# Kernel tuning notes

Measured on AMD Instinct MI355X. Metric: run time of the kernel, lower is better.

Reference implementation:

```python
import jax, jax.numpy as jnp
import numpy as np

B, H, W = 8, 384, 384
KH = KW = 3
STRIDE, PAD = 1, 1


def setup_inputs() -> dict:
    key = jax.random.key(0)
    ks = jax.random.split(key, 5)
    pf = jax.random.normal(ks[0], (B, 3, H, W), jnp.float32)
    cf = jax.random.normal(ks[1], (B, 3, H, W), jnp.float32)
    mv = jax.random.normal(ks[2], (B, 2, H, W), jnp.float32)
    offset_w = jax.random.normal(ks[3], (18, 8, KH, KW), jnp.float32) * 0.05
    offset_b = jnp.zeros((18,), jnp.float32)
    deform_w = jax.random.normal(ks[4], (3, 3, KH, KW), jnp.float32) * 0.1
    return dict(pf=pf, cf=cf, mv=mv, offset_w=offset_w, offset_b=offset_b, deform_w=deform_w)


def _conv2d(x, w, b):
    y = jax.lax.conv_general_dilated(
        x, w, window_strides=(STRIDE, STRIDE),
        padding=((PAD, PAD), (PAD, PAD)),
        dimension_numbers=('NCHW', 'OIHW', 'NCHW'))
    return y + b[None, :, None, None]


def _deform_conv2d(x, offset, w):
    # x: [B, Cin, H, W]; offset: [B, 2*KH*KW, Ho, Wo] (torchvision order: per tap k -> (dy, dx))
    Bn, Cin, Hn, Wn = x.shape
    Ho, Wo = offset.shape[2], offset.shape[3]
    K = KH * KW
    off = offset.reshape(Bn, K, 2, Ho, Wo)
    ky = jnp.repeat(jnp.arange(KH), KW).astype(x.dtype)   # [K] kernel row offset
    kx = jnp.tile(jnp.arange(KW), KH).astype(x.dtype)     # [K] kernel col offset
    base_y = (jnp.arange(Ho) * STRIDE - PAD).astype(x.dtype)
    base_x = (jnp.arange(Wo) * STRIDE - PAD).astype(x.dtype)
    # sampling positions p = p0 + p_k + delta_p_k, shape [B, K, Ho, Wo]
    py = off[:, :, 0] + ky[None, :, None, None] + base_y[None, None, :, None]
    px = off[:, :, 1] + kx[None, :, None, None] + base_x[None, None, None, :]
    y0 = jnp.floor(py)
    x0 = jnp.floor(px)
    wy = py - y0  # bilinear weights, [B, K, Ho, Wo]
    wx = px - x0

    def gather(yi, xi):
        # zero padding outside the image (torchvision semantics)
        valid = (yi >= 0) & (yi < Hn) & (xi >= 0) & (xi < Wn)
        yc = jnp.clip(yi, 0, Hn - 1).astype(jnp.int32)
        xc = jnp.clip(xi, 0, Wn - 1).astype(jnp.int32)
        v = jax.vmap(lambda im, y, xg: im[:, y, xg])(x, yc, xc)  # [B, Cin, K, Ho, Wo]
        return v * valid[:, None].astype(x.dtype)

    v00 = gather(y0, x0)
    v01 = gather(y0, x0 + 1)
    v10 = gather(y0 + 1, x0)
    v11 = gather(y0 + 1, x0 + 1)
    wy_ = wy[:, None]  # broadcast over channel dim
    wx_ = wx[:, None]
    samp = (v00 * (1 - wy_) * (1 - wx_) + v01 * (1 - wy_) * wx_
            + v10 * wy_ * (1 - wx_) + v11 * wy_ * wx_)  # [B, Cin, K, Ho, Wo]
    # weighted accumulation over taps and input channels (no bias)
    return jnp.einsum('oik,bikhw->bohw', w.reshape(w.shape[0], w.shape[1], K), samp)


def reference(pf, cf, mv, offset_w, offset_b, deform_w):
    x = jnp.concatenate([pf, cf, mv], axis=1)          # [B, 8, H, W]
    offset = _conv2d(x, offset_w, offset_b)            # [B, 18, H, W]
    return _deform_conv2d(pf, offset, deform_w)        # [B, 3, H, W]
```

## Files before the change

kernel.cpp:

```cpp
#include <hip/hip_runtime.h>


#define Bn 8
#define Hn 384
#define Wn 384
#define HWn (Hn * Wn)
#define TILE 16
#define PH 4
#define PT 24

#define OFF_PTILE 0
#define SZ_PTILE (PT * PT * 2)
#define OFF_T8   SZ_PTILE
#define SZ_T8U   4864
#define SMEM_FLOATS (OFF_T8 + SZ_T8U)

typedef float f32x4 __attribute__((ext_vector_type(4)));
typedef float f32x2 __attribute__((ext_vector_type(2)));
typedef unsigned u32x2 __attribute__((ext_vector_type(2)));
typedef short s16x8 __attribute__((ext_vector_type(8)));

static __device__ inline f32x2 vfma2(f32x2 a, f32x2 b, f32x2 c) {
#if __has_builtin(__builtin_elementwise_fma)
    return __builtin_elementwise_fma(a, b, c);
#else
    f32x2 r; r.x = fmaf(a.x, b.x, c.x); r.y = fmaf(a.y, b.y, c.y); return r;
#endif
}
static __device__ inline f32x2 vfloor2(f32x2 a) {
#if __has_builtin(__builtin_elementwise_floor)
    return __builtin_elementwise_floor(a);
#else
    f32x2 r; r.x = floorf(a.x); r.y = floorf(a.y); return r;
#endif
}
static __device__ inline f32x2 splat2(float s) {
    f32x2 r; r.x = s; r.y = s; return r;
}

__device__ inline unsigned short rne_bf16(float f) {
    unsigned u = __float_as_uint(f);
    u += 0x7fffu + ((u >> 16) & 1u);
    return (unsigned short)(u >> 16);
}

__global__ void prep_bw(const float* __restrict__ ow, unsigned short* __restrict__ bwg) {
    const int idx = blockIdx.x * 64 + threadIdx.x;
    const int sg   = idx >> 6;
    const int lane = idx & 63;
    const int s  = sg >> 1;
    const int nt = sg & 1;
    const int am = lane & 15;
    const int g  = lane >> 4;
    const int oc = nt * 16 + am;
    const int t  = 4 * s + g;
    union { unsigned short h[8]; s16x8 v; } F;
#pragma unroll
    for (int c = 0; c < 8; ++c) {
        float w = 0.f;
        if (t < 9 && oc < 18) w = ow[oc * 72 + c * 9 + t];
        F.h[c] = rne_bf16(w);
    }
    ((s16x8*)bwg)[idx] = F.v;
}

__global__ __launch_bounds__(256, 6) void guided_cnn_fused(
    const float* __restrict__ pf, const float* __restrict__ cf,
    const float* __restrict__ mv, const s16x8* __restrict__ bwg,
    const float* __restrict__ ob, const float* __restrict__ dw,
    float* __restrict__ out)
{
    __shared__ float smem[SMEM_FLOATS];

    const int tid = threadIdx.x;
    const int b = blockIdx.z;
    const int tileY0 = blockIdx.y * TILE;
    const int tileX0 = blockIdx.x * TILE;
    const int oy = tileY0 - PH;
    const int ox = tileX0 - PH;

    unsigned* ptileB = (unsigned*)(smem + OFF_PTILE);
    float* t8b = smem + OFF_T8;

    const int lane = tid & 63;
    const int wv   = tid >> 6;
    const int am   = lane & 15;
    const int g    = lane >> 4;

    s16x8 bfrag[3][2];
#pragma unroll
    for (int s = 0; s < 3; ++s)
#pragma unroll
        for (int nt = 0; nt < 2; ++nt)
            bfrag[s][nt] = bwg[(s * 2 + nt) * 64 + lane];

    const float bias0 = ob[am];
    const float bias1 = ob[am < 2 ? 16 + am : 17];

    for (int p = tid; p < PT * PT; p += 256) {
        const int row = p / PT;
        const int col = p - row * PT;
        const int gy = oy + row, gx = ox + col;
        const bool v = ((unsigned)gy < (unsigned)Hn) && ((unsigned)gx < (unsigned)Wn);
        const size_t gidx = (size_t)b * 3 * HWn + gy * Wn + gx;
        const float v0 = v ? pf[gidx] : 0.f;
        const float v1 = v ? pf[gidx + HWn] : 0.f;
        const float v2 = v ? pf[gidx + 2 * HWn] : 0.f;
        u32x2 q;
        q.x = (unsigned)rne_bf16(v0) | ((unsigned)rne_bf16(v1) << 16);
        q.y = (unsigned)rne_bf16(v2);
        *(u32x2*)(ptileB + p * 2) = q;
    }
    for (int p = tid; p < 324; p += 256) {
        const int row = p / 18;
        const int col = p - row * 18;
        const int gy = tileY0 + row - 1, gx = tileX0 + col - 1;
        const bool v = ((unsigned)gy < (unsigned)Hn) && ((unsigned)gx < (unsigned)Wn);
        const size_t base = (size_t)b * 3 * HWn + gy * Wn + gx;
        float c0 = v ? pf[base] : 0.f;
        float c1 = v ? pf[base + HWn] : 0.f;
        float c2 = v ? pf[base + 2 * HWn] : 0.f;
        float c3 = v ? cf[base] : 0.f;
        float c4 = v ? cf[base + HWn] : 0.f;
        float c5 = v ? cf[base + 2 * HWn] : 0.f;
        const size_t mbase = (size_t)b * 2 * HWn + gy * Wn + gx;
        float c6 = v ? mv[mbase] : 0.f;
        float c7 = v ? mv[mbase + HWn] : 0.f;
        union { unsigned u[4]; f32x4 f; } P;
        P.u[0] = (unsigned)rne_bf16(c0) | ((unsigned)rne_bf16(c1) << 16);
        P.u[1] = (unsigned)rne_bf16(c2) | ((unsigned)rne_bf16(c3) << 16);
        P.u[2] = (unsigned)rne_bf16(c4) | ((unsigned)rne_bf16(c5) << 16);
        P.u[3] = (unsigned)rne_bf16(c6) | ((unsigned)rne_bf16(c7) << 16);
        *(f32x4*)(t8b + p * 4) = P.f;
    }
    __syncthreads();

    f32x4 acc[4][2];
#pragma unroll
    for (int mt = 0; mt < 4; ++mt) {
        acc[mt][0] = (f32x4){bias0, bias0, bias0, bias0};
        acc[mt][1] = (f32x4){bias1, bias1, bias1, bias1};
    }

#pragma unroll
    for (int mt = 0; mt < 4; ++mt) {
        const int mrow = wv * 4 + mt;
#pragma unroll
        for (int s = 0; s < 3; ++s) {
            const int tap = 4 * s + g;
            const int tc  = tap < 9 ? tap : 8;
            const int dy = tc / 3, dx = tc - dy * 3;
            union { f32x4 f; s16x8 v; } A;
            A.f = *(const f32x4*)(t8b + ((mrow + dy) * 18 + (am + dx)) * 4);
            acc[mt][0] = __builtin_amdgcn_mfma_f32_16x16x32_bf16(A.v, bfrag[s][0], acc[mt][0], 0, 0, 0);
            acc[mt][1] = __builtin_amdgcn_mfma_f32_16x16x32_bf16(A.v, bfrag[s][1], acc[mt][1], 0, 0, 0);
        }
    }
    __syncthreads();

    float* offb = smem + OFF_T8;
#pragma unroll
    for (int mt = 0; mt < 4; ++mt) {
        const int prow = wv * 4 + mt;
#pragma unroll
        for (int r = 0; r < 4; ++r) {
            const int pix = prow * 16 + (g * 4 + r);
            offb[pix * 19 + am] = acc[mt][0][r];
            if (am < 2) offb[pix * 19 + 16 + am] = acc[mt][1][r];
        }
    }
    __syncthreads();

    const int tx = tid & 15;
    const int ty = tid >> 4;
    const int x = tileX0 + tx;
    const int y = tileY0 + ty;

    f32x2 offs2[9];
#pragma unroll
    for (int j = 0; j < 9; ++j) {
        offs2[j].x = offb[tid * 19 + 2 * j];
        offs2[j].y = offb[tid * 19 + 2 * j + 1];
    }

    const float* p0 = pf + (size_t)b * 3 * HWn;
    f32x2 accP = splat2(0.f);
    float acc2c = 0.f;
    const float tyf = (float)(ty + PH - 1);
    const float txf = (float)(tx + PH - 1);

#pragma unroll
    for (int k = 0; k < 9; ++k) {
        const int ky = k / 3;
        const int kx = k - ky * 3;
        f32x2 basek;
        basek.x = tyf + (float)ky;
        basek.y = txf + (float)kx;
        const f32x2 pyx = offs2[k] + basek;
        const f32x2 fl = vfloor2(pyx);
        const f32x2 w  = pyx - fl;
        const int ty0 = (int)fl.x;
        const int tx0 = (int)fl.y;
        const float wy = w.x, wx = w.y;

        const bool inT = ((unsigned)ty0 < (unsigned)(PT - 1)) &&
                         ((unsigned)tx0 < (unsigned)(PT - 1));
        float s0, s1, s2;
        if (inT) {
            const int pix = ty0 * PT + tx0;
            const u32x2 r00 = *(const u32x2*)(ptileB + pix * 2);
            const u32x2 r01 = *(const u32x2*)(ptileB + (pix + 1) * 2);
            const u32x2 r10 = *(const u32x2*)(ptileB + (pix + PT) * 2);
            const u32x2 r11 = *(const u32x2*)(ptileB + (pix + PT + 1) * 2);
            f32x2 q00; q00.x = __uint_as_float(r00.x << 16);
                       q00.y = __uint_as_float(r00.x & 0xffff0000u);
            f32x2 q01; q01.x = __uint_as_float(r01.x << 16);
                       q01.y = __uint_as_float(r01.x & 0xffff0000u);
            f32x2 q10; q10.x = __uint_as_float(r10.x << 16);
                       q10.y = __uint_as_float(r10.x & 0xffff0000u);
            f32x2 q11; q11.x = __uint_as_float(r11.x << 16);
                       q11.y = __uint_as_float(r11.x & 0xffff0000u);
            const float a2 = __uint_as_float(r00.y << 16);
            const float b2 = __uint_as_float(r01.y << 16);
            const float c2 = __uint_as_float(r10.y << 16);
            const float d2 = __uint_as_float(r11.y << 16);
            const f32x2 wx2 = splat2(wx);
            const f32x2 wy2 = splat2(wy);
            const f32x2 h0 = vfma2(wx2, q01 - q00, q00);
            const f32x2 h1 = vfma2(wx2, q11 - q10, q10);
            const f32x2 s01 = vfma2(wy2, h1 - h0, h0);
            const float h0c = fmaf(wx, b2 - a2, a2);
            const float h1c = fmaf(wx, d2 - c2, c2);
            s0 = s01.x; s1 = s01.y;
            s2 = fmaf(wy, h1c - h0c, h0c);
        } else {
            const int y0 = ty0 + oy, x0 = tx0 + ox;
            const int y1 = y0 + 1,  x1 = x0 + 1;
            const bool vy0 = ((unsigned)y0 < (unsigned)Hn);
            const bool vy1 = ((unsigned)y1 < (unsigned)Hn);
            const bool vx0 = ((unsigned)x0 < (unsigned)Wn);
            const bool vx1 = ((unsigned)x1 < (unsigned)Wn);
            const int y0c = min(max(y0, 0), Hn - 1);
            const int y1c = min(max(y1, 0), Hn - 1);
            const int x0c = min(max(x0, 0), Wn - 1);
            const int x1c = min(max(x1, 0), Wn - 1);
            const int i00 = y0c * Wn + x0c;
            const int i01 = y0c * Wn + x1c;
            const int i10 = y1c * Wn + x0c;
            const int i11 = y1c * Wn + x1c;
            const float w00 = (1.f - wy) * (1.f - wx);
            const float w01 = (1.f - wy) * wx;
            const float w10 = wy * (1.f - wx);
            const float w11 = wy * wx;
            float sv[3];
#pragma unroll
            for (int i = 0; i < 3; ++i) {
                const float* pl = p0 + (size_t)i * HWn;
                const float v00 = (vy0 && vx0) ? pl[i00] : 0.f;
                const float v01 = (vy0 && vx1) ? pl[i01] : 0.f;
                const float v10 = (vy1 && vx0) ? pl[i10] : 0.f;
                const float v11 = (vy1 && vx1) ? pl[i11] : 0.f;
                sv[i] = w00 * v00 + w01 * v01 + w10 * v10 + w11 * v11;
            }
            s0 = sv[0]; s1 = sv[1]; s2 = sv[2];
        }
        {
            f32x2 dwp0; dwp0.x = dw[0 * 27 + 0 * 9 + k]; dwp0.y = dw[1 * 27 + 0 * 9 + k];
            f32x2 dwp1; dwp1.x = dw[0 * 27 + 1 * 9 + k]; dwp1.y = dw[1 * 27 + 1 * 9 + k];
            f32x2 dwp2; dwp2.x = dw[0 * 27 + 2 * 9 + k]; dwp2.y = dw[1 * 27 + 2 * 9 + k];
            accP = vfma2(dwp0, splat2(s0), accP);
            accP = vfma2(dwp1, splat2(s1), accP);
            accP = vfma2(dwp2, splat2(s2), accP);
            acc2c = fmaf(dw[2 * 27 + 0 * 9 + k], s0, acc2c);
            acc2c = fmaf(dw[2 * 27 + 1 * 9 + k], s1, acc2c);
            acc2c = fmaf(dw[2 * 27 + 2 * 9 + k], s2, acc2c);
        }
    }

    const size_t obase = ((size_t)b * 3 * Hn + y) * Wn + x;
    out[obase] = accP.x;
    out[obase + HWn] = accP.y;
    out[obase + 2 * HWn] = acc2c;
}

extern "C" void kernel_launch(void* const* d_in, const int* in_sizes, int n_in,
                              void* d_out, int out_size, void* d_ws, size_t ws_size,
                              hipStream_t stream) {
    const float* pf = (const float*)d_in[0];
    const float* cf = (const float*)d_in[1];
    const float* mv = (const float*)d_in[2];
    const float* ow = (const float*)d_in[3];
    const float* ob = (const float*)d_in[4];
    const float* dw = (const float*)d_in[5];
    float* out = (float*)d_out;
    unsigned short* bwg = (unsigned short*)d_ws;

    prep_bw<<<6, 64, 0, stream>>>(ow, bwg);
    dim3 grid(Wn / TILE, Hn / TILE, Bn);
    guided_cnn_fused<<<grid, 256, 0, stream>>>(pf, cf, mv, (const s16x8*)bwg, ob, dw, out);
}
```

Before: 117.2 us.

## Store offsets as fp16 in tap-major LDS, raise occupancy, remap grid

The computed offset field is now stored in shared memory as packed fp16 pairs in a tap-major layout with a padded stride. This shrinks the LDS footprint from 4864 to 2313 floats and gives conflict-free per-thread reads. The launch bound rises from 6 to 8 blocks per CU. The grid is flattened to 1D with the batch index in the low bits, so neighbouring blocks work on different images at the same spatial tile. Rounding offsets to fp16 loses precision in the bilinear sampling positions, which can matter at large coordinates, and the tighter register budget may cause spills.

```diff
diff --git a/kernel.cpp b/kernel.cpp
--- a/kernel.cpp
+++ b/kernel.cpp
@@ -1,4 +1,5 @@
 #include <hip/hip_runtime.h>
+#include <hip/hip_fp16.h>
 
 
 #define Bn 8
@@ -8,11 +9,12 @@
 #define TILE 16
 #define PH 4
 #define PT 24
+#define OSTR 257
 
 #define OFF_PTILE 0
 #define SZ_PTILE (PT * PT * 2)
 #define OFF_T8   SZ_PTILE
-#define SZ_T8U   4864
+#define SZ_T8U   (9 * OSTR)
 #define SMEM_FLOATS (OFF_T8 + SZ_T8U)
 
 typedef float f32x4 __attribute__((ext_vector_type(4)));
@@ -42,6 +44,16 @@
     unsigned u = __float_as_uint(f);
     u += 0x7fffu + ((u >> 16) & 1u);
     return (unsigned short)(u >> 16);
+}
+static __device__ inline unsigned short f32_to_f16u(float f) {
+    union { __half h; unsigned short u; } c;
+    c.h = __float2half(f);
+    return c.u;
+}
+static __device__ inline float f16u_to_f32(unsigned short u) {
+    union { __half h; unsigned short u; } c;
+    c.u = u;
+    return __half2float(c.h);
 }
 
 __global__ void prep_bw(const float* __restrict__ ow, unsigned short* __restrict__ bwg) {
@@ -64,7 +76,7 @@
     ((s16x8*)bwg)[idx] = F.v;
 }
 
-__global__ __launch_bounds__(256, 6) void guided_cnn_fused(
+__global__ __launch_bounds__(256, 8) void guided_cnn_fused(
     const float* __restrict__ pf, const float* __restrict__ cf,
     const float* __restrict__ mv, const s16x8* __restrict__ bwg,
     const float* __restrict__ ob, const float* __restrict__ dw,
@@ -73,9 +85,13 @@
     __shared__ float smem[SMEM_FLOATS];
 
     const int tid = threadIdx.x;
-    const int b = blockIdx.z;
-    const int tileY0 = blockIdx.y * TILE;
-    const int tileX0 = blockIdx.x * TILE;
+    const int bid = blockIdx.x;
+    const int b  = bid & 7;
+    const int sp = bid >> 3;
+    const int byi = sp / 24;
+    const int bxi = sp - byi * 24;
+    const int tileY0 = byi * TILE;
+    const int tileX0 = bxi * TILE;
     const int oy = tileY0 - PH;
     const int ox = tileX0 - PH;
 
@@ -158,15 +174,18 @@
     }
     __syncthreads();
 
-    float* offb = smem + OFF_T8;
+    unsigned short* offh = (unsigned short*)(smem + OFF_T8);
+    const int tap0 = am >> 1;
+    const int cmp0 = am & 1;
 #pragma unroll
     for (int mt = 0; mt < 4; ++mt) {
         const int prow = wv * 4 + mt;
 #pragma unroll
         for (int r = 0; r < 4; ++r) {
             const int pix = prow * 16 + (g * 4 + r);
-            offb[pix * 19 + am] = acc[mt][0][r];
-            if (am < 2) offb[pix * 19 + 16 + am] = acc[mt][1][r];
+            offh[(tap0 * OSTR + pix) * 2 + cmp0] = f32_to_f16u(acc[mt][0][r]);
+            if (am < 2)
+                offh[(8 * OSTR + pix) * 2 + am] = f32_to_f16u(acc[mt][1][r]);
         }
     }
     __syncthreads();
@@ -176,11 +195,13 @@
     const int x = tileX0 + tx;
     const int y = tileY0 + ty;
 
+    const unsigned* offp = (const unsigned*)(smem + OFF_T8);
     f32x2 offs2[9];
 #pragma unroll
-    for (int j = 0; j < 9; ++j) {
-        offs2[j].x = offb[tid * 19 + 2 * j];
-        offs2[j].y = offb[tid * 19 + 2 * j + 1];
+    for (int t = 0; t < 9; ++t) {
+        const unsigned w = offp[t * OSTR + tid];
+        offs2[t].x = f16u_to_f32((unsigned short)(w & 0xffffu));
+        offs2[t].y = f16u_to_f32((unsigned short)(w >> 16));
     }
 
     const float* p0 = pf + (size_t)b * 3 * HWn;
@@ -296,6 +317,5 @@
     unsigned short* bwg = (unsigned short*)d_ws;
 
     prep_bw<<<6, 64, 0, stream>>>(ow, bwg);
-    dim3 grid(Wn / TILE, Hn / TILE, Bn);
-    guided_cnn_fused<<<grid, 256, 0, stream>>>(pf, cf, mv, (const s16x8*)bwg, ob, dw, out);
-}
+    guided_cnn_fused<<<4608, 256, 0, stream>>>(pf, cf, mv, (const s16x8*)bwg, ob, dw, out);
+}
```

After: 167.2 us. 1.43x slower.
